# Performance work log

Measured on AMD Instinct MI355X. Metric: run time of the kernel, lower is better.

Reference implementation:

```python
import jax, jax.numpy as jnp
import numpy as np

B, S, D = 2, 2048, 2048
N_HEADS, N_KV_HEADS, HEAD_DIM = 16, 8, 128
N_REP = N_HEADS // N_KV_HEADS
EPS = 1e-6
SCALE = HEAD_DIM ** -0.5


def setup_inputs() -> dict:
    key = jax.random.key(0)
    ks = jax.random.split(key, 6)
    x = jax.random.normal(ks[0], (B, S, D), dtype=jnp.float32)
    # RoPE frequencies (Llama-style cis stored as interleaved [cos, sin])
    inv_freq = 1.0 / (1e6 ** (jnp.arange(0, HEAD_DIM, 2, dtype=jnp.float32) / HEAD_DIM))
    angles = jnp.arange(S, dtype=jnp.float32)[:, None] * inv_freq[None, :]  # [S, HEAD_DIM//2]
    freqs_cis = jnp.stack([jnp.cos(angles), jnp.sin(angles)], axis=-1)  # [S, HEAD_DIM//2, 2]
    wq = jax.random.normal(ks[1], (N_HEADS * HEAD_DIM, D), dtype=jnp.float32) * 0.02
    wk = jax.random.normal(ks[2], (N_KV_HEADS * HEAD_DIM, D), dtype=jnp.float32) * 0.02
    wv = jax.random.normal(ks[3], (N_KV_HEADS * HEAD_DIM, D), dtype=jnp.float32) * 0.02
    wo = jax.random.normal(ks[4], (D, N_HEADS * HEAD_DIM), dtype=jnp.float32) * 0.02
    q_norm_w = jnp.ones((HEAD_DIM,), dtype=jnp.float32)
    k_norm_w = jnp.ones((HEAD_DIM,), dtype=jnp.float32)
    return {"x": x, "freqs_cis": freqs_cis, "wq": wq, "wk": wk, "wv": wv,
            "wo": wo, "q_norm_w": q_norm_w, "k_norm_w": k_norm_w}


def _rmsnorm(t, w):
    var = jnp.mean(jnp.square(t), axis=-1, keepdims=True)
    return t * jax.lax.rsqrt(var + EPS) * w


def _apply_rope(t, cos, sin):
    # t: [B, S, H, HEAD_DIM]; cos/sin: [1, S, 1, HEAD_DIM//2]
    tp = t.reshape(*t.shape[:-1], HEAD_DIM // 2, 2)
    tr, ti = tp[..., 0], tp[..., 1]
    out = jnp.stack([tr * cos - ti * sin, tr * sin + ti * cos], axis=-1)
    return out.reshape(t.shape)


def reference(x, freqs_cis, wq, wk, wv, wo, q_norm_w, k_norm_w):
    bs, seqlen, _ = x.shape
    xq = (x @ wq.T).reshape(bs, seqlen, N_HEADS, HEAD_DIM)
    xk = (x @ wk.T).reshape(bs, seqlen, N_KV_HEADS, HEAD_DIM)
    xv = (x @ wv.T).reshape(bs, seqlen, N_KV_HEADS, HEAD_DIM)
    # per-head RMSNorm (Qwen3)
    xq = _rmsnorm(xq, q_norm_w)
    xk = _rmsnorm(xk, k_norm_w)
    # rotary embedding
    cos = freqs_cis[:seqlen, :, 0][None, :, None, :]
    sin = freqs_cis[:seqlen, :, 1][None, :, None, :]
    xq = _apply_rope(xq, cos, sin)
    xk = _apply_rope(xk, cos, sin)
    # GQA: repeat kv heads
    keys = jnp.repeat(xk, N_REP, axis=2)    # [B, S, N_HEADS, HEAD_DIM]
    values = jnp.repeat(xv, N_REP, axis=2)
    q = xq.transpose(0, 2, 1, 3)   # [B, H, S, D]
    k = keys.transpose(0, 2, 1, 3)
    v = values.transpose(0, 2, 1, 3)
    scores = jnp.einsum("bhqd,bhkd->bhqk", q, k) * SCALE
    causal = jnp.tril(jnp.ones((seqlen, seqlen), dtype=bool))
    scores = jnp.where(causal[None, None], scores, jnp.finfo(scores.dtype).min)
    attn = jax.nn.softmax(scores, axis=-1)
    out = jnp.einsum("bhqk,bhkd->bhqd", attn, v)
    out = out.transpose(0, 2, 1, 3).reshape(bs, seqlen, N_HEADS * HEAD_DIM)
    return out @ wo.T
```

## Files before the change

kernel.cpp:

```cpp
#include <hip/hip_runtime.h>

#define B_ 2
#define S_ 2048
#define D_ 2048
#define NH 16
#define NKV 8
#define HD 128
#define SCALE 0.08838834764831845f
#define CEXP 0.1275255f
#define RTHR 62.733f

typedef unsigned short u16;
typedef __attribute__((ext_vector_type(8))) short short8;
typedef __attribute__((ext_vector_type(4))) float f32x4;
typedef __attribute__((ext_vector_type(16))) float f32x16;
typedef __attribute__((ext_vector_type(4))) int i32x4;
typedef __attribute__((ext_vector_type(2))) int i32x2;

#define ASM_VMCNT(N) asm volatile("s_waitcnt vmcnt(" #N ")" ::: "memory")
#define MEMFENCE asm volatile("" ::: "memory")

__device__ __forceinline__ u16 f2b(float f) {
  union { float f; unsigned u; } c; c.f = f;
  unsigned u = c.u;
  return (u16)((u + 0x7fffu + ((u >> 16) & 1u)) >> 16);
}
__device__ __forceinline__ float b2f(u16 h) {
  union { unsigned u; float f; } c; c.u = ((unsigned)h) << 16;
  return c.f;
}
__device__ __forceinline__ float exp2f_fast(float x) {
  float r; asm("v_exp_f32 %0, %1" : "=v"(r) : "v"(x)); return r;
}
__device__ __forceinline__ int cvtpk(float a, float b) {
  int r; asm("v_cvt_pk_bf16_f32 %0, %1, %2" : "=v"(r) : "v"(a), "v"(b)); return r;
}
__device__ __forceinline__ void pl32swap(int& a, int& b) {
  asm volatile("v_permlane32_swap_b32 %0, %1" : "+v"(a), "+v"(b));
}

__device__ __forceinline__ void load_lds16(const u16* g, u16* l) {
  __builtin_amdgcn_global_load_lds(
      (const __attribute__((address_space(1))) unsigned int*)g,
      (__attribute__((address_space(3))) unsigned int*)l, 16, 0, 0);
}

__global__ __launch_bounds__(256) void cvt_all(const float* __restrict__ x,
                                               const float* __restrict__ wq,
                                               const float* __restrict__ wk,
                                               const float* __restrict__ wv,
                                               const float* __restrict__ wo,
                                               u16* __restrict__ xb,
                                               u16* __restrict__ wqkvb,
                                               u16* __restrict__ wob) {
  const int blk = blockIdx.x;
  const float* src; u16* dst; int base;
  if (blk < 8192)       { src = x;  dst = xb;                  base = blk; }
  else if (blk < 12288) { src = wq; dst = wqkvb;               base = blk - 8192; }
  else if (blk < 14336) { src = wk; dst = wqkvb + 2048 * 2048; base = blk - 12288; }
  else if (blk < 16384) { src = wv; dst = wqkvb + 3072 * 2048; base = blk - 14336; }
  else                  { src = wo; dst = wob;                 base = blk - 16384; }
  int i = base * 256 + threadIdx.x;
  float4 v = ((const float4*)src)[i];
  u16 o0 = f2b(v.x), o1 = f2b(v.y), o2 = f2b(v.z), o3 = f2b(v.w);
  unsigned long long packed = (unsigned long long)o0 | ((unsigned long long)o1 << 16) |
                              ((unsigned long long)o2 << 32) | ((unsigned long long)o3 << 48);
  ((unsigned long long*)dst)[i] = packed;
}

#define LDA4Q(dst, SRC) \
  { _Pragma("unroll") for (int i2 = 0; i2 < 4; ++i2) { \
      const int arow = wr * 64 + i2 * 16 + r; \
      dst[i2] = *(const short8*)&(SRC)[arow * 32 + ((hi ^ ((arow >> 1) & 3)) << 3)]; } }
#define LDB4Q(dst, SRC) \
  { _Pragma("unroll") for (int n2 = 0; n2 < 4; ++n2) { \
      const int brow = wc * 64 + n2 * 16 + r; \
      dst[n2] = *(const short8*)&(SRC)[brow * 32 + ((hi ^ ((brow >> 1) & 3)) << 3)]; } }
#define MFMA16Q(AF, BF) \
  { __builtin_amdgcn_s_setprio(1); \
    _Pragma("unroll") for (int i2 = 0; i2 < 4; ++i2) \
    _Pragma("unroll") for (int n2 = 0; n2 < 4; ++n2) \
      acc[i2][n2] = __builtin_amdgcn_mfma_f32_16x16x32_bf16(AF[i2], BF[n2], acc[i2][n2], 0, 0, 0); \
    __builtin_amdgcn_s_setprio(0); }

__global__ __launch_bounds__(512, 4) void gemm_qkv_fused(const u16* __restrict__ A,
                                                         const u16* __restrict__ Bm,
                                                         const float* __restrict__ fc,
                                                         const float* __restrict__ qw,
                                                         const float* __restrict__ kw,
                                                         u16* __restrict__ qrope,
                                                         u16* __restrict__ krope,
                                                         u16* __restrict__ vt) {
  __shared__ __align__(16) u16 As2[2][8192];
  __shared__ __align__(16) u16 Bs2[2][4096];
  __shared__ float sq[2][256];
  const int tid = threadIdx.x;
  const int wave = tid >> 6, lane = tid & 63;
  const int L = (blockIdx.x & 7) * 64 + (blockIdx.x >> 3);
  const int bm = L >> 5, bn = L & 31;
  const int wr = wave >> 1, wc = wave & 1;
  const int r = lane & 15, hi = lane >> 4;
  const int rowA0 = bm * 256, rowB0 = bn * 128;

  f32x4 acc[4][4];
#pragma unroll
  for (int mi = 0; mi < 4; ++mi)
#pragma unroll
    for (int ni = 0; ni < 4; ++ni) acc[mi][ni] = (f32x4){0.f, 0.f, 0.f, 0.f};

  auto stage_ha = [&](u16* lds, int kcol) {
#pragma unroll
    for (int l = 0; l < 2; ++l) {
      const int p = wave * 2048 + l * 1024 + lane * 16;
      const int row = p >> 6, slot = (p >> 4) & 3;
      const int kg = slot ^ ((row >> 1) & 3);
      load_lds16(A + (size_t)(rowA0 + row) * 2048 + kcol + kg * 8,
                 lds + ((wave * 2048 + l * 1024) >> 1));
    }
  };
  auto stage_hb = [&](u16* lds, int kcol) {
    const int p = wave * 1024 + lane * 16;
    const int row = p >> 6, slot = (p >> 4) & 3;
    const int kg = slot ^ ((row >> 1) & 3);
    load_lds16(Bm + (size_t)(rowB0 + row) * 2048 + kcol + kg * 8,
               lds + ((wave * 1024) >> 1));
  };

  for (int kt = 0; kt < 32; ++kt) {
    const int k0 = kt << 6;
    stage_ha(As2[0], k0);
    stage_hb(Bs2[0], k0);
    stage_ha(As2[1], k0 + 32);
    stage_hb(Bs2[1], k0 + 32);
    ASM_VMCNT(0);
    __builtin_amdgcn_s_barrier();
    MEMFENCE;
    short8 af[4], bf[4];
    LDB4Q(bf, Bs2[0]); LDA4Q(af, As2[0]);
    MFMA16Q(af, bf);
    LDB4Q(bf, Bs2[1]); LDA4Q(af, As2[1]);
    MFMA16Q(af, bf);
    MEMFENCE;
    __builtin_amdgcn_s_barrier();
  }

  if (bn >= 24) {
    const int hv = bn - 24;
#pragma unroll
    for (int mi = 0; mi < 4; ++mi) {
      const int tok0 = bm * 256 + wr * 64 + mi * 16 + hi * 4;
      const int bb = tok0 >> 11, sl = tok0 & 2047;
#pragma unroll
      for (int ni = 0; ni < 4; ++ni) {
        const int d = wc * 64 + ni * 16 + r;
        int w0 = cvtpk(acc[mi][ni][0], acc[mi][ni][1]);
        int w1 = cvtpk(acc[mi][ni][2], acc[mi][ni][3]);
        i32x2 pk = (i32x2){w0, w1};
        *(i32x2*)(vt + ((size_t)(bb * 8 + hv) * 128 + d) * 2048 + sl) = pk;
      }
    }
  } else {
    const float* nw = (bn < 16) ? qw : kw;
    float nwv[4];
#pragma unroll
    for (int ni = 0; ni < 4; ++ni) nwv[ni] = nw[wc * 64 + ni * 16 + r];
    float ssq[4][4];
#pragma unroll
    for (int mi = 0; mi < 4; ++mi)
#pragma unroll
      for (int r2 = 0; r2 < 4; ++r2) {
        float s4 = 0.f;
#pragma unroll
        for (int ni = 0; ni < 4; ++ni) {
          float a = acc[mi][ni][r2];
          s4 = __builtin_fmaf(a, a, s4);
        }
#pragma unroll
        for (int mk = 1; mk < 16; mk <<= 1) s4 += __shfl_xor(s4, mk, 64);
        ssq[mi][r2] = s4;
      }
    if (r == 0) {
#pragma unroll
      for (int mi = 0; mi < 4; ++mi)
#pragma unroll
        for (int r2 = 0; r2 < 4; ++r2)
          sq[wc][wr * 64 + mi * 16 + hi * 4 + r2] = ssq[mi][r2];
    }
    __syncthreads();
    u16* outp = (bn < 16) ? qrope : krope;
#pragma unroll
    for (int mi = 0; mi < 4; ++mi) {
      const int tok0 = bm * 256 + wr * 64 + mi * 16 + hi * 4;
      const int bb = tok0 >> 11;
      const size_t headbase = (bn < 16) ? ((size_t)(bb * 16 + bn) * 2048)
                                        : ((size_t)(bb * 8 + (bn - 16)) * 2048);
#pragma unroll
      for (int r2 = 0; r2 < 4; ++r2) {
        const int sl = (tok0 + r2) & 2047;
        const float tot = ssq[mi][r2] + sq[wc ^ 1][wr * 64 + mi * 16 + hi * 4 + r2];
        const float rms = rsqrtf(tot * (1.0f / 128.0f) + 1e-6f);
#pragma unroll
        for (int ni = 0; ni < 4; ++ni) {
          const int d = wc * 64 + ni * 16 + r;
          float val = acc[mi][ni][r2] * rms * nwv[ni];
          float prt = __shfl_xor(val, 1, 64);
          const float2 cs = *(const float2*)&fc[(size_t)(sl * 64 + (d >> 1)) * 2];
          float outv = (r & 1) ? (prt * cs.y + val * cs.x)
                               : (val * cs.x - prt * cs.y);
          outp[(headbase + sl) * 128 + d] = f2b(outv);
        }
      }
    }
  }
}

template<int OUTF32>
__global__ __launch_bounds__(256, 4) void gemm_bt3(const u16* __restrict__ A, const u16* __restrict__ Bm,
                                                   void* __restrict__ Cv, int M, int N, int K, int nbn) {
  __shared__ __align__(16) u16 As[128 * 64];
  __shared__ __align__(16) u16 Bs[128 * 64];
  const int tid = threadIdx.x;
  const int wave = tid >> 6, lane = tid & 63;
  const int nwg = gridDim.x, cpx = nwg >> 3;
  const int L = (blockIdx.x & 7) * cpx + (blockIdx.x >> 3);
  const int bm = L / nbn, bn = L % nbn;
  const int wr = wave >> 1, wc = wave & 1;
  const int r = lane & 15, hi = lane >> 4;

  f32x4 acc[4][4];
#pragma unroll
  for (int m = 0; m < 4; ++m)
#pragma unroll
    for (int n = 0; n < 4; ++n) acc[m][n] = (f32x4){0.f, 0.f, 0.f, 0.f};

  const int gslot = (lane & 7) ^ (lane >> 3);
  const int srow = lane >> 3;

  auto stage = [&](int k0) {
#pragma unroll
    for (int jj = 0; jj < 4; ++jj) {
      int j = wave * 4 + jj;
      int row = j * 8 + srow;
      load_lds16(A + (size_t)(bm * 128 + row) * K + k0 + gslot * 8, &As[j * 512]);
      load_lds16(Bm + (size_t)(bn * 128 + row) * K + k0 + gslot * 8, &Bs[j * 512]);
    }
  };

  const int nk = K >> 6;
  for (int kt = 0; kt < nk; ++kt) {
    stage(kt << 6);
    ASM_VMCNT(0);
    __builtin_amdgcn_s_barrier();
    MEMFENCE;
#pragma unroll
    for (int kc = 0; kc < 2; ++kc) {
      short8 af[4], bfr[4];
#pragma unroll
      for (int m = 0; m < 4; ++m) {
        int row = wr * 64 + m * 16 + r;
        int slot = (hi + kc * 4) ^ (row & 7);
        af[m] = *(const short8*)&As[row * 64 + slot * 8];
      }
#pragma unroll
      for (int n = 0; n < 4; ++n) {
        int row = wc * 64 + n * 16 + r;
        int slot = (hi + kc * 4) ^ (row & 7);
        bfr[n] = *(const short8*)&Bs[row * 64 + slot * 8];
      }
#pragma unroll
      for (int m = 0; m < 4; ++m)
#pragma unroll
        for (int n = 0; n < 4; ++n)
          acc[m][n] = __builtin_amdgcn_mfma_f32_16x16x32_bf16(af[m], bfr[n], acc[m][n], 0, 0, 0);
    }
    MEMFENCE;
    __builtin_amdgcn_s_barrier();
  }

#pragma unroll
  for (int m = 0; m < 4; ++m)
#pragma unroll
    for (int n = 0; n < 4; ++n)
#pragma unroll
      for (int r2 = 0; r2 < 4; ++r2) {
        int grow = bm * 128 + wr * 64 + m * 16 + hi * 4 + r2;
        int gcol = bn * 128 + wc * 64 + n * 16 + r;
        if (OUTF32)
          ((float*)Cv)[(size_t)grow * N + gcol] = acc[m][n][r2];
        else
          ((u16*)Cv)[(size_t)grow * N + gcol] = f2b(acc[m][n][r2]);
      }
}

__global__ __launch_bounds__(256, 2) void attn9(const u16* __restrict__ qr, const u16* __restrict__ kr,
                                                const u16* __restrict__ vt, u16* __restrict__ ao) {
  __shared__ __align__(16) u16 Ks[2][64 * 128];
  __shared__ __align__(16) u16 Vs[2][128 * 64];
  const int tid = threadIdx.x, wave = tid >> 6, lane = tid & 63;
  const int ql = lane & 31, lh = lane >> 5;

  const int blk = blockIdx.x;
  const int half = blk >> 8;
  const int xcd = blk & 7;
  const int idx = (blk >> 3) & 31;
  const int bh = xcd * 4 + (idx & 3);
  const int pp = idx >> 2;
  const int t = half ? pp : 15 - pp;
  const int b = bh >> 4, h = bh & 15, hkv = h >> 1;

  const u16* Q  = qr + (size_t)(b * 16 + h) * S_ * HD;
  const u16* Kg = kr + (size_t)(b * 8 + hkv) * S_ * HD;
  const u16* Vg = vt + (size_t)(b * 8 + hkv) * HD * S_;

  const int q0w = t * 128 + wave * 32;
  const int nsteps = 2 * (t + 1);

  short8 qf[8];
#pragma unroll
  for (int ki = 0; ki < 8; ++ki)
    qf[ki] = *(const short8*)(Q + (size_t)(q0w + ql) * HD + ki * 16 + lh * 8);

  f32x16 o[4];
#pragma unroll
  for (int dt = 0; dt < 4; ++dt) o[dt] = 0.f;
  float m = -1e30f, l = 0.f;

  auto stage = [&](int buf, int kv0) {
#pragma unroll
    for (int inst = 0; inst < 4; ++inst) {
      int pp2 = wave * 4096 + inst * 1024 + lane * 16;
      int row = pp2 >> 8;
      int colb = (pp2 & 255) ^ ((row & 7) << 4);
      load_lds16(Kg + (((size_t)(kv0 + row)) << 7) + (colb >> 1),
                 &Ks[buf][(wave * 4096 + inst * 1024) >> 1]);
    }
#pragma unroll
    for (int inst = 0; inst < 4; ++inst) {
      int pp2 = wave * 4096 + inst * 1024 + lane * 16;
      int d = pp2 >> 7;
      int colb = (pp2 & 127) ^ ((d & 7) << 4);
      load_lds16(Vg + (size_t)d * S_ + kv0 + (colb >> 1),
                 &Vs[buf][(wave * 4096 + inst * 1024) >> 1]);
    }
  };

  stage(0, 0);
  for (int i = 0; i < nsteps; ++i) {
    const int kv0 = i * 64;
    const u16* kb = Ks[i & 1];
    const u16* vb = Vs[i & 1];

    ASM_VMCNT(0);
    __builtin_amdgcn_s_barrier();
    MEMFENCE;
    if (i + 1 < nsteps) stage((i + 1) & 1, kv0 + 64);

    if (kv0 < q0w + 32) {
      f32x16 sacc[2];
      sacc[0] = 0.f; sacc[1] = 0.f;
      __builtin_amdgcn_s_setprio(1);
#pragma unroll
      for (int ki = 0; ki < 8; ++ki) {
        const int off = ki * 32 + lh * 16;
#pragma unroll
        for (int kvt = 0; kvt < 2; ++kvt) {
          const int row = kvt * 32 + ql;
          short8 kf = *(const short8*)&kb[(row << 7) + ((off ^ ((row & 7) << 4)) >> 1)];
          sacc[kvt] = __builtin_amdgcn_mfma_f32_32x32x16_bf16(kf, qf[ki], sacc[kvt], 0, 0, 0);
        }
      }
      __builtin_amdgcn_s_setprio(0);
      const int q = q0w + ql;
      if (kv0 + 64 > q0w) {
#pragma unroll
        for (int kvt = 0; kvt < 2; ++kvt) {
          const int kvb = kv0 + kvt * 32 + 4 * lh;
#pragma unroll
          for (int reg = 0; reg < 16; ++reg) {
            const int kvr = kvb + (reg & 3) + 8 * (reg >> 2);
            sacc[kvt][reg] = (kvr > q) ? -1e30f : sacc[kvt][reg];
          }
        }
      }
      float mx = sacc[0][0];
#pragma unroll
      for (int kvt = 0; kvt < 2; ++kvt)
#pragma unroll
        for (int reg = 0; reg < 16; ++reg) mx = fmaxf(mx, sacc[kvt][reg]);
      mx = fmaxf(mx, __shfl_xor(mx, 32, 64));
      if (__any(mx > m + RTHR)) {
        float mn = fmaxf(m, mx);
        float sc = exp2f_fast((m - mn) * CEXP);
        l *= sc;
        m = mn;
#pragma unroll
        for (int dt = 0; dt < 4; ++dt)
#pragma unroll
          for (int reg = 0; reg < 16; ++reg) o[dt][reg] *= sc;
      }
      short8 pf[4];
      const float mc = m * CEXP;
      float ps = 0.f;
#pragma unroll
      for (int kvt = 0; kvt < 2; ++kvt) {
        float pv[16];
#pragma unroll
        for (int reg = 0; reg < 16; ++reg) {
          pv[reg] = exp2f_fast(__builtin_fmaf(sacc[kvt][reg], CEXP, -mc));
          ps += pv[reg];
        }
        int A0 = cvtpk(pv[0], pv[1]),  B0 = cvtpk(pv[2], pv[3]);
        int C0 = cvtpk(pv[4], pv[5]),  D0 = cvtpk(pv[6], pv[7]);
        int A1 = cvtpk(pv[8], pv[9]),  B1 = cvtpk(pv[10], pv[11]);
        int C1 = cvtpk(pv[12], pv[13]), D1 = cvtpk(pv[14], pv[15]);
        pl32swap(A0, C0);
        pl32swap(B0, D0);
        pl32swap(A1, C1);
        pl32swap(B1, D1);
        i32x4 w0 = (i32x4){A0, B0, C0, D0};
        i32x4 w1 = (i32x4){A1, B1, C1, D1};
        pf[kvt * 2]     = *(short8*)&w0;
        pf[kvt * 2 + 1] = *(short8*)&w1;
      }
      l += ps;
      __builtin_amdgcn_s_setprio(1);
#pragma unroll
      for (int kc = 0; kc < 4; ++kc) {
        const int off = kc * 32 + lh * 16;
#pragma unroll
        for (int dt = 0; dt < 4; ++dt) {
          const int d = dt * 32 + ql;
          short8 vf = *(const short8*)&vb[(d << 6) + ((off ^ ((d & 7) << 4)) >> 1)];
          o[dt] = __builtin_amdgcn_mfma_f32_32x32x16_bf16(vf, pf[kc], o[dt], 0, 0, 0);
        }
      }
      __builtin_amdgcn_s_setprio(0);
    }
    MEMFENCE;
  }

  l += __shfl_xor(l, 32, 64);
  const float inv = 1.0f / l;
  const size_t rowoff = ((size_t)(b * 2048 + q0w + ql)) * 2048 + h * 128;
#pragma unroll
  for (int dt = 0; dt < 4; ++dt)
#pragma unroll
    for (int g = 0; g < 4; ++g) {
      const int d0 = dt * 32 + 8 * g + 4 * lh;
      int w0 = cvtpk(o[dt][4 * g] * inv, o[dt][4 * g + 1] * inv);
      int w1 = cvtpk(o[dt][4 * g + 2] * inv, o[dt][4 * g + 3] * inv);
      i32x2 pk = (i32x2){w0, w1};
      *(i32x2*)((u16*)ao + rowoff + d0) = pk;
    }
}

extern "C" void kernel_launch(void* const* d_in, const int* in_sizes, int n_in,
                              void* d_out, int out_size, void* d_ws, size_t ws_size,
                              hipStream_t stream) {
  const float* x = (const float*)d_in[0];
  const float* fc = (const float*)d_in[1];
  const float* wq = (const float*)d_in[2];
  const float* wk = (const float*)d_in[3];
  const float* wv = (const float*)d_in[4];
  const float* wo = (const float*)d_in[5];
  const float* qw = (const float*)d_in[6];
  const float* kw = (const float*)d_in[7];
  float* out = (float*)d_out;
  char* ws = (char*)d_ws;

  u16* xb    = (u16*)(ws);
  u16* wqkvb = (u16*)(ws + 16777216);
  u16* wob   = (u16*)(ws + 33554432);
  u16* qrope = (u16*)(ws + 75497472);
  u16* krope = (u16*)(ws + 92274688);
  u16* vtb   = (u16*)(ws + 100663296);
  u16* ao    = (u16*)(ws + 109051904);

  cvt_all<<<20480, 256, 0, stream>>>(x, wq, wk, wv, wo, xb, wqkvb, wob);

  gemm_qkv_fused<<<512, 512, 0, stream>>>(xb, wqkvb, fc, qw, kw, qrope, krope, vtb);

  attn9<<<512, 256, 0, stream>>>(qrope, krope, vtb, ao);

  gemm_bt3<1><<<512, 256, 0, stream>>>(ao, wob, (void*)out, 4096, 2048, 2048, 16);
}
```

Baseline: 193.4 us.

## Prefetch next K-tile into registers during MFMA in QKV projection GEMM

```diff
diff --git a/kernel.cpp b/kernel.cpp
--- a/kernel.cpp
+++ b/kernel.cpp
@@ -18,6 +18,7 @@
 typedef __attribute__((ext_vector_type(2))) int i32x2;
 
 #define ASM_VMCNT(N) asm volatile("s_waitcnt vmcnt(" #N ")" ::: "memory")
+#define ASM_LGKM0 asm volatile("s_waitcnt lgkmcnt(0)" ::: "memory")
 #define MEMFENCE asm volatile("" ::: "memory")
 
 __device__ __forceinline__ u16 f2b(float f) {
@@ -108,32 +109,65 @@
 #pragma unroll
     for (int ni = 0; ni < 4; ++ni) acc[mi][ni] = (f32x4){0.f, 0.f, 0.f, 0.f};
 
-  auto stage_ha = [&](u16* lds, int kcol) {
-#pragma unroll
-    for (int l = 0; l < 2; ++l) {
-      const int p = wave * 2048 + l * 1024 + lane * 16;
-      const int row = p >> 6, slot = (p >> 4) & 3;
-      const int kg = slot ^ ((row >> 1) & 3);
-      load_lds16(A + (size_t)(rowA0 + row) * 2048 + kcol + kg * 8,
-                 lds + ((wave * 2048 + l * 1024) >> 1));
-    }
-  };
-  auto stage_hb = [&](u16* lds, int kcol) {
+  const u16* gA[4];
+  const u16* gB[2];
+  unsigned ldsA[4], ldsB[2];
+#pragma unroll
+  for (int l = 0; l < 2; ++l) {
+    const int p = wave * 2048 + l * 1024 + lane * 16;
+    const int row = p >> 6, slot = (p >> 4) & 3;
+    const int kg = slot ^ ((row >> 1) & 3);
+    gA[l] = A + (size_t)(rowA0 + row) * 2048 + kg * 8;
+    gA[2 + l] = gA[l];
+    ldsA[l] = p;
+    ldsA[2 + l] = p;
+  }
+  {
     const int p = wave * 1024 + lane * 16;
     const int row = p >> 6, slot = (p >> 4) & 3;
     const int kg = slot ^ ((row >> 1) & 3);
-    load_lds16(Bm + (size_t)(rowB0 + row) * 2048 + kcol + kg * 8,
-               lds + ((wave * 1024) >> 1));
+    gB[0] = Bm + (size_t)(rowB0 + row) * 2048 + kg * 8;
+    gB[1] = gB[0];
+    ldsB[0] = p;
+    ldsB[1] = p;
+  }
+
+  i32x4 pA[4], pB[2];
+  auto pf_load = [&](int kcol) {
+#pragma unroll
+    for (int l = 0; l < 2; ++l) {
+      pA[l]     = *(const i32x4*)(gA[l] + kcol);
+      pA[2 + l] = *(const i32x4*)(gA[l] + kcol + 32);
+    }
+    pB[0] = *(const i32x4*)(gB[0] + kcol);
+    pB[1] = *(const i32x4*)(gB[0] + kcol + 32);
   };
+  auto pf_write = [&]() {
+#pragma unroll
+    for (int l = 0; l < 2; ++l) {
+      *(i32x4*)((char*)&As2[0][0] + ldsA[l]) = pA[l];
+      *(i32x4*)((char*)&As2[1][0] + ldsA[l]) = pA[2 + l];
+    }
+    *(i32x4*)((char*)&Bs2[0][0] + ldsB[0]) = pB[0];
+    *(i32x4*)((char*)&Bs2[1][0] + ldsB[0]) = pB[1];
+  };
+
+  {
+#pragma unroll
+    for (int l = 0; l < 2; ++l) {
+      load_lds16(gA[l],      (u16*)((char*)&As2[0][0] + (ldsA[l] & ~1023u)));
+      load_lds16(gA[l] + 32, (u16*)((char*)&As2[1][0] + (ldsA[l] & ~1023u)));
+    }
+    load_lds16(gB[0],      (u16*)((char*)&Bs2[0][0] + (ldsB[0] & ~1023u)));
+    load_lds16(gB[0] + 32, (u16*)((char*)&Bs2[1][0] + (ldsB[0] & ~1023u)));
+  }
+  ASM_VMCNT(0);
+  __builtin_amdgcn_s_barrier();
+  MEMFENCE;
 
   for (int kt = 0; kt < 32; ++kt) {
-    const int k0 = kt << 6;
-    stage_ha(As2[0], k0);
-    stage_hb(Bs2[0], k0);
-    stage_ha(As2[1], k0 + 32);
-    stage_hb(Bs2[1], k0 + 32);
-    ASM_VMCNT(0);
-    __builtin_amdgcn_s_barrier();
+    const bool hn = kt + 1 < 32;
+    if (hn) pf_load((kt + 1) << 6);
     MEMFENCE;
     short8 af[4], bf[4];
     LDB4Q(bf, Bs2[0]); LDA4Q(af, As2[0]);
@@ -142,6 +176,13 @@
     MFMA16Q(af, bf);
     MEMFENCE;
     __builtin_amdgcn_s_barrier();
+    if (hn) {
+      ASM_VMCNT(0);
+      pf_write();
+      ASM_LGKM0;
+    }
+    __builtin_amdgcn_s_barrier();
+    MEMFENCE;
   }
 
   if (bn >= 24) {
```

Measured after the change: 202.4 us. 1.05x slower.

## Shrink QKV GEMM tile to 128x128 with 4 waves and XOR-swizzled 64-wide LDS

Applied to the files above, without the earlier changes.

```diff
diff --git a/kernel.cpp b/kernel.cpp
--- a/kernel.cpp
+++ b/kernel.cpp
@@ -68,39 +68,23 @@
   ((unsigned long long*)dst)[i] = packed;
 }
 
-#define LDA4Q(dst, SRC) \
-  { _Pragma("unroll") for (int i2 = 0; i2 < 4; ++i2) { \
-      const int arow = wr * 64 + i2 * 16 + r; \
-      dst[i2] = *(const short8*)&(SRC)[arow * 32 + ((hi ^ ((arow >> 1) & 3)) << 3)]; } }
-#define LDB4Q(dst, SRC) \
-  { _Pragma("unroll") for (int n2 = 0; n2 < 4; ++n2) { \
-      const int brow = wc * 64 + n2 * 16 + r; \
-      dst[n2] = *(const short8*)&(SRC)[brow * 32 + ((hi ^ ((brow >> 1) & 3)) << 3)]; } }
-#define MFMA16Q(AF, BF) \
-  { __builtin_amdgcn_s_setprio(1); \
-    _Pragma("unroll") for (int i2 = 0; i2 < 4; ++i2) \
-    _Pragma("unroll") for (int n2 = 0; n2 < 4; ++n2) \
-      acc[i2][n2] = __builtin_amdgcn_mfma_f32_16x16x32_bf16(AF[i2], BF[n2], acc[i2][n2], 0, 0, 0); \
-    __builtin_amdgcn_s_setprio(0); }
-
-__global__ __launch_bounds__(512, 4) void gemm_qkv_fused(const u16* __restrict__ A,
-                                                         const u16* __restrict__ Bm,
-                                                         const float* __restrict__ fc,
-                                                         const float* __restrict__ qw,
-                                                         const float* __restrict__ kw,
-                                                         u16* __restrict__ qrope,
-                                                         u16* __restrict__ krope,
-                                                         u16* __restrict__ vt) {
-  __shared__ __align__(16) u16 As2[2][8192];
-  __shared__ __align__(16) u16 Bs2[2][4096];
-  __shared__ float sq[2][256];
+__global__ __launch_bounds__(256, 4) void gemm_qkv_fused2(const u16* __restrict__ A,
+                                                          const u16* __restrict__ Bm,
+                                                          const float* __restrict__ fc,
+                                                          const float* __restrict__ qw,
+                                                          const float* __restrict__ kw,
+                                                          u16* __restrict__ qrope,
+                                                          u16* __restrict__ krope,
+                                                          u16* __restrict__ vt) {
+  __shared__ __align__(16) u16 As[128 * 64];
+  __shared__ __align__(16) u16 Bs[128 * 64];
+  __shared__ float sq[2][128];
   const int tid = threadIdx.x;
   const int wave = tid >> 6, lane = tid & 63;
-  const int L = (blockIdx.x & 7) * 64 + (blockIdx.x >> 3);
+  const int L = (blockIdx.x & 7) * 128 + (blockIdx.x >> 3);
   const int bm = L >> 5, bn = L & 31;
   const int wr = wave >> 1, wc = wave & 1;
   const int r = lane & 15, hi = lane >> 4;
-  const int rowA0 = bm * 256, rowB0 = bn * 128;
 
   f32x4 acc[4][4];
 #pragma unroll
@@ -108,38 +92,47 @@
 #pragma unroll
     for (int ni = 0; ni < 4; ++ni) acc[mi][ni] = (f32x4){0.f, 0.f, 0.f, 0.f};
 
-  auto stage_ha = [&](u16* lds, int kcol) {
-#pragma unroll
-    for (int l = 0; l < 2; ++l) {
-      const int p = wave * 2048 + l * 1024 + lane * 16;
-      const int row = p >> 6, slot = (p >> 4) & 3;
-      const int kg = slot ^ ((row >> 1) & 3);
-      load_lds16(A + (size_t)(rowA0 + row) * 2048 + kcol + kg * 8,
-                 lds + ((wave * 2048 + l * 1024) >> 1));
+  const int gslot = (lane & 7) ^ (lane >> 3);
+  const int srow = lane >> 3;
+
+  auto stage = [&](int k0) {
+#pragma unroll
+    for (int jj = 0; jj < 4; ++jj) {
+      int j = wave * 4 + jj;
+      int row = j * 8 + srow;
+      load_lds16(A + (size_t)(bm * 128 + row) * 2048 + k0 + gslot * 8, &As[j * 512]);
+      load_lds16(Bm + (size_t)(bn * 128 + row) * 2048 + k0 + gslot * 8, &Bs[j * 512]);
     }
   };
-  auto stage_hb = [&](u16* lds, int kcol) {
-    const int p = wave * 1024 + lane * 16;
-    const int row = p >> 6, slot = (p >> 4) & 3;
-    const int kg = slot ^ ((row >> 1) & 3);
-    load_lds16(Bm + (size_t)(rowB0 + row) * 2048 + kcol + kg * 8,
-               lds + ((wave * 1024) >> 1));
-  };
 
   for (int kt = 0; kt < 32; ++kt) {
-    const int k0 = kt << 6;
-    stage_ha(As2[0], k0);
-    stage_hb(Bs2[0], k0);
-    stage_ha(As2[1], k0 + 32);
-    stage_hb(Bs2[1], k0 + 32);
+    stage(kt << 6);
     ASM_VMCNT(0);
     __builtin_amdgcn_s_barrier();
     MEMFENCE;
-    short8 af[4], bf[4];
-    LDB4Q(bf, Bs2[0]); LDA4Q(af, As2[0]);
-    MFMA16Q(af, bf);
-    LDB4Q(bf, Bs2[1]); LDA4Q(af, As2[1]);
-    MFMA16Q(af, bf);
+#pragma unroll
+    for (int kc = 0; kc < 2; ++kc) {
+      short8 af[4], bfr[4];
+#pragma unroll
+      for (int m = 0; m < 4; ++m) {
+        int row = wr * 64 + m * 16 + r;
+        int slot = (hi + kc * 4) ^ (row & 7);
+        af[m] = *(const short8*)&As[row * 64 + slot * 8];
+      }
+#pragma unroll
+      for (int n = 0; n < 4; ++n) {
+        int row = wc * 64 + n * 16 + r;
+        int slot = (hi + kc * 4) ^ (row & 7);
+        bfr[n] = *(const short8*)&Bs[row * 64 + slot * 8];
+      }
+      __builtin_amdgcn_s_setprio(1);
+#pragma unroll
+      for (int m = 0; m < 4; ++m)
+#pragma unroll
+        for (int n = 0; n < 4; ++n)
+          acc[m][n] = __builtin_amdgcn_mfma_f32_16x16x32_bf16(af[m], bfr[n], acc[m][n], 0, 0, 0);
+      __builtin_amdgcn_s_setprio(0);
+    }
     MEMFENCE;
     __builtin_amdgcn_s_barrier();
   }
@@ -148,7 +141,7 @@
     const int hv = bn - 24;
 #pragma unroll
     for (int mi = 0; mi < 4; ++mi) {
-      const int tok0 = bm * 256 + wr * 64 + mi * 16 + hi * 4;
+      const int tok0 = bm * 128 + wr * 64 + mi * 16 + hi * 4;
       const int bb = tok0 >> 11, sl = tok0 & 2047;
 #pragma unroll
       for (int ni = 0; ni < 4; ++ni) {
@@ -190,7 +183,7 @@
     u16* outp = (bn < 16) ? qrope : krope;
 #pragma unroll
     for (int mi = 0; mi < 4; ++mi) {
-      const int tok0 = bm * 256 + wr * 64 + mi * 16 + hi * 4;
+      const int tok0 = bm * 128 + wr * 64 + mi * 16 + hi * 4;
       const int bb = tok0 >> 11;
       const size_t headbase = (bn < 16) ? ((size_t)(bb * 16 + bn) * 2048)
                                         : ((size_t)(bb * 8 + (bn - 16)) * 2048);
@@ -478,7 +471,7 @@
 
   cvt_all<<<20480, 256, 0, stream>>>(x, wq, wk, wv, wo, xb, wqkvb, wob);
 
-  gemm_qkv_fused<<<512, 512, 0, stream>>>(xb, wqkvb, fc, qw, kw, qrope, krope, vtb);
+  gemm_qkv_fused2<<<1024, 256, 0, stream>>>(xb, wqkvb, fc, qw, kw, qrope, krope, vtb);
 
   attn9<<<512, 256, 0, stream>>>(qrope, krope, vtb, ao);
 
```

After: 199.5 us. 1.03x slower.
